# Kernel optimization log

Measured on AMD Instinct MI355X. Metric: run time of the kernel, lower is better.

The kernel has to match this reference:

```python
import jax, jax.numpy as jnp
import numpy as np

B, L, HID = 2, 2048, 4096
NH, NKV, HD = 16, 4, 64
BLOCK = 16
THETA = 8000000.0
EPS = 1e-6
NEG = jnp.finfo(jnp.float32).min


def _rope_tables(theta, L, hd):
    inv_freq = 1.0 / (theta ** (np.arange(0, hd, 2, dtype=np.float32) / hd))  # [hd/2]
    t = np.arange(L, dtype=np.float32)
    freqs = np.outer(t, inv_freq)                      # [L, hd/2]
    emb = np.concatenate([freqs, freqs], axis=-1)      # [L, hd]
    return jnp.asarray(np.cos(emb)), jnp.asarray(np.sin(emb))


def setup_inputs() -> dict:
    key = jax.random.key(0)
    k1, k2, k3 = jax.random.split(key, 3)
    hidden_states = jax.random.normal(k1, (B, L, HID), dtype=jnp.float32)
    Wqkv = jax.random.normal(k2, (HID, (NH + 2 * NKV) * HD), dtype=jnp.float32) * 0.006
    Wo = jax.random.normal(k3, (NH * HD, HID), dtype=jnp.float32) * 0.006
    q_norm_w = jnp.ones((HD,), dtype=jnp.float32)
    k_norm_w = jnp.ones((HD,), dtype=jnp.float32)
    # block-diagonal causal additive mask [1,1,L,L]
    idx = jnp.arange(L)
    same_block = (idx[:, None] // BLOCK) == (idx[None, :] // BLOCK)
    causal = idx[:, None] >= idx[None, :]
    attention_mask = jnp.where(same_block & causal, 0.0, NEG)[None, None].astype(jnp.float32)
    cos1, sin1 = _rope_tables(THETA, L, HD)
    cos = jnp.broadcast_to(cos1[None], (B, L, HD))
    sin = jnp.broadcast_to(sin1[None], (B, L, HD))
    return {"hidden_states": hidden_states, "attention_mask": attention_mask,
            "cos": cos, "sin": sin, "Wqkv": Wqkv, "Wo": Wo,
            "q_norm_w": q_norm_w, "k_norm_w": k_norm_w}


def _rms_norm(x, w):
    xf = x.astype(jnp.float32)
    var = jnp.mean(xf * xf, axis=-1, keepdims=True)
    return (xf * jax.lax.rsqrt(var + EPS)).astype(x.dtype) * w


def _rotate_half(x):
    x1, x2 = jnp.split(x, 2, axis=-1)
    return jnp.concatenate([-x2, x1], axis=-1)


def reference(hidden_states, attention_mask, cos, sin, Wqkv, Wo, q_norm_w, k_norm_w):
    Bc, Lc, _ = hidden_states.shape
    qkv = hidden_states @ Wqkv                                # [B,L,(NH+2NKV)*HD]
    qkv = qkv.reshape(Bc, Lc, NH + 2 * NKV, HD)
    q, k, v = jnp.split(qkv, [NH, NH + NKV], axis=2)
    q = q.transpose(0, 2, 1, 3)                               # [B,NH,L,HD]
    k = k.transpose(0, 2, 1, 3)                               # [B,NKV,L,HD]
    v = v.transpose(0, 2, 1, 3)
    q = _rms_norm(q, q_norm_w)
    k = _rms_norm(k, k_norm_w)
    c = cos[:, None]                                          # [B,1,L,HD]
    s = sin[:, None]
    q = q * c + _rotate_half(q) * s
    k = k * c + _rotate_half(k) * s
    groups = NH // NKV
    k = jnp.repeat(k, groups, axis=1)                         # [B,NH,L,HD]
    v = jnp.repeat(v, groups, axis=1)
    scale = 1.0 / jnp.sqrt(jnp.float32(HD))
    scores = jnp.einsum('bhqd,bhkd->bhqk', q, k) * scale + attention_mask
    probs = jax.nn.softmax(scores, axis=-1)
    out = jnp.einsum('bhqk,bhkd->bhqd', probs, v)             # [B,NH,L,HD]
    out = out.transpose(0, 2, 1, 3).reshape(Bc, Lc, NH * HD)
    return out @ Wo
```

## Files before the change

### kernel.cpp

```cpp
#include <hip/hip_runtime.h>
#include <hip/hip_bf16.h>
#include <cstdint>

#define B_SZ   2
#define L_SEQ  2048
#define HID    4096
#define NH     16
#define NKV    4
#define HD     64
#define NQKV   (NH + 2*NKV)
#define QKV_N  (NQKV*HD)
#define O_N    (NH*HD)
#define M_ROWS (B_SZ*L_SEQ)
#define EPSV   1e-6f

typedef __bf16  bf16x8_t  __attribute__((ext_vector_type(8)));
typedef float   f32x4_t   __attribute__((ext_vector_type(4)));
typedef unsigned short ushort8_t __attribute__((ext_vector_type(8)));

__device__ __forceinline__ unsigned short f2b(float f) {
    union { float f; uint32_t u; } v; v.f = f;
    uint32_t r = v.u + 0x7FFFu + ((v.u >> 16) & 1u);
    return (unsigned short)(r >> 16);
}
__device__ __forceinline__ float b2f(unsigned short u) {
    union { uint32_t u; float f; } v; v.u = ((uint32_t)u) << 16;
    return v.f;
}

__device__ __forceinline__ void gload_lds16(const void* g, void* l) {
    __builtin_amdgcn_global_load_lds(
        (__attribute__((address_space(1))) void*)(g),
        (__attribute__((address_space(3))) void*)(l),
        16, 0, 0);
}

#define BARF() do { asm volatile("" ::: "memory"); \
                    __builtin_amdgcn_s_barrier();  \
                    asm volatile("" ::: "memory"); } while (0)
#define LGKMW() asm volatile("s_waitcnt lgkmcnt(0)" ::: "memory")

template <int N> __device__ __forceinline__ void vmcnt_wait() {
    if constexpr (N == 4)       asm volatile("s_waitcnt vmcnt(4)"  ::: "memory");
    else if constexpr (N == 5)  asm volatile("s_waitcnt vmcnt(5)"  ::: "memory");
    else if constexpr (N == 6)  asm volatile("s_waitcnt vmcnt(6)"  ::: "memory");
    else if constexpr (N == 8)  asm volatile("s_waitcnt vmcnt(8)"  ::: "memory");
    else if constexpr (N == 12) asm volatile("s_waitcnt vmcnt(12)" ::: "memory");
    else                        asm volatile("s_waitcnt vmcnt(0)"  ::: "memory");
}

__global__ __launch_bounds__(256) void cvt_f32_bf16(const float* __restrict__ in,
                                                    unsigned short* __restrict__ out,
                                                    int n8) {
    int i = blockIdx.x * 256 + threadIdx.x;
    if (i >= n8) return;
    const float4* p = (const float4*)(in + (size_t)i * 8);
    float4 a = p[0], b = p[1];
    ushort8_t o;
    o[0]=f2b(a.x); o[1]=f2b(a.y); o[2]=f2b(a.z); o[3]=f2b(a.w);
    o[4]=f2b(b.x); o[5]=f2b(b.y); o[6]=f2b(b.z); o[7]=f2b(b.w);
    *(ushort8_t*)(out + (size_t)i * 8) = o;
}

__global__ __launch_bounds__(256) void transpose_both(const float* __restrict__ Wqkv,
                                                      unsigned short* __restrict__ WqkvT,
                                                      const float* __restrict__ Wo,
                                                      unsigned short* __restrict__ WoT) {
    __shared__ float t[32][33];
    const float* in;
    unsigned short* out;
    int R, C, bx, by;
    if (blockIdx.x < 6144) {
        in = Wqkv; out = WqkvT; R = HID; C = QKV_N;
        bx = blockIdx.x % 48; by = blockIdx.x / 48;
    } else {
        int b = blockIdx.x - 6144;
        in = Wo; out = WoT; R = O_N; C = HID;
        bx = b % 128; by = b / 128;
    }
    const int c0 = bx * 32;
    const int r0 = by * 32;
    const int tx = threadIdx.x & 31;
    const int ty = threadIdx.x >> 5;
    #pragma unroll
    for (int i = 0; i < 32; i += 8)
        t[ty + i][tx] = in[(size_t)(r0 + ty + i) * C + c0 + tx];
    __syncthreads();
    #pragma unroll
    for (int i = 0; i < 32; i += 8)
        out[(size_t)(c0 + ty + i) * R + r0 + tx] = f2b(t[tx][ty + i]);
}

template <int BM, int BN, int BK, int NBUF, int NWM, int NWN, bool OBF16, typename OutT>
__global__ __launch_bounds__(512, 2)
void gemm_sb(const unsigned short* __restrict__ A,
             const unsigned short* __restrict__ Bt,
             OutT* __restrict__ C, int M, int N, int K) {
    constexpr int WM    = BM / NWM;
    constexpr int WN    = BN / NWN;
    constexpr int AF    = WM / 16;
    constexpr int BF    = WN / 16;
    constexpr int KK    = BK / 32;
    constexpr int BUF   = (BM + BN) * BK;
    constexpr int ROWS  = 4096 / BK;
    constexpr int AR    = BM / ROWS;
    constexpr int BR    = BN / ROWS;
    constexpr int RNDS  = AR + BR;
    constexpr int DEPTH = NBUF - 2;

    __shared__ unsigned short smem[NBUF * BUF];

    const int tid  = threadIdx.x;
    const int lane = tid & 63;
    const int wave = tid >> 6;
    const int wm   = wave / NWN;
    const int wn   = wave % NWN;
    const int fr   = lane & 15;
    const int fq   = lane >> 4;

    const int nbx = N / BN;
    int bid = blockIdx.x;
    const int cpx = gridDim.x >> 3;
    bid = (bid & 7) * cpx + (bid >> 3);
    const int bx = bid % nbx, by = bid / nbx;
    const int m0 = by * BM, n0 = bx * BN;

    const int srow = tid / (BK / 8);
    const int sch  = tid & (BK / 8 - 1);
    const int ssw  = (BK == 64) ? (srow & 7) : ((srow >> 1) & 3);
    const int scs  = (sch ^ ssw) << 3;
    const unsigned short* gA = A  + (size_t)(m0 + srow) * K + scs;
    const unsigned short* gB = Bt + (size_t)(n0 + srow) * K + scs;

    const int frsw = (BK == 64) ? (fr & 7) : ((fr >> 1) & 3);

    f32x4_t acc[AF][BF];
    #pragma unroll
    for (int m = 0; m < AF; m++)
        #pragma unroll
        for (int n = 0; n < BF; n++)
            acc[m][n] = (f32x4_t){0.f, 0.f, 0.f, 0.f};

    const int NT = K / BK;

    auto STAGE = [&](int T) {
        const int pb = (T % NBUF) * BUF;
        #pragma unroll
        for (int q = 0; q < AR; ++q)
            gload_lds16(gA + (size_t)(q * ROWS) * K + (size_t)T * BK,
                        &smem[pb + q * 4096 + tid * 8]);
        #pragma unroll
        for (int q = 0; q < BR; ++q)
            gload_lds16(gB + (size_t)(q * ROWS) * K + (size_t)T * BK,
                        &smem[pb + BM * BK + q * 4096 + tid * 8]);
    };

    #pragma unroll
    for (int pt = 0; pt < NBUF - 1; ++pt) STAGE(pt);
    vmcnt_wait<DEPTH * RNDS>();

    for (int t = 0; t < NT; ++t) {
        const int sb = (t % NBUF) * BUF;
        BARF();

        #pragma unroll
        for (int kk = 0; kk < KK; ++kk) {
            const int cxk = (((kk * 4 + fq) ^ frsw)) << 3;
            bf16x8_t aF[AF], bF[BF];
            #pragma unroll
            for (int mm = 0; mm < AF; ++mm)
                aF[mm] = *(const bf16x8_t*)&smem[sb + (wm*WM + mm*16 + fr)*BK + cxk];
            #pragma unroll
            for (int nn = 0; nn < BF; ++nn)
                bF[nn] = *(const bf16x8_t*)&smem[sb + BM*BK + (wn*WN + nn*16 + fr)*BK + cxk];

            if (kk == 0 && t + NBUF - 1 < NT) STAGE(t + NBUF - 1);

            __builtin_amdgcn_s_setprio(1);
            #pragma unroll
            for (int mm = 0; mm < AF; ++mm)
                #pragma unroll
                for (int nn = 0; nn < BF; ++nn)
                    acc[mm][nn] = __builtin_amdgcn_mfma_f32_16x16x32_bf16(
                        aF[mm], bF[nn], acc[mm][nn], 0, 0, 0);
            __builtin_amdgcn_s_setprio(0);
        }

        if constexpr (DEPTH == 2) {
            if (t + 3 < NT)      { vmcnt_wait<2 * RNDS>(); }
            else if (t + 2 < NT) { vmcnt_wait<RNDS>(); }
            else if (t + 1 < NT) { vmcnt_wait<0>(); }
        } else {
            if (t + 2 < NT)      { vmcnt_wait<RNDS>(); }
            else if (t + 1 < NT) { vmcnt_wait<0>(); }
        }
    }

    const int crow = m0 + wm * WM + fq * 4;
    const int ccol = n0 + wn * WN + fr;
    #pragma unroll
    for (int m = 0; m < AF; m++)
        #pragma unroll
        for (int n = 0; n < BF; n++)
            #pragma unroll
            for (int rr = 0; rr < 4; rr++) {
                const size_t idx = (size_t)(crow + m*16 + rr) * N + ccol + n*16;
                if constexpr (OBF16) C[idx] = (OutT)f2b(acc[m][n][rr]);
                else                 C[idx] = (OutT)acc[m][n][rr];
            }
}

#define G2_BUF 32768

__global__ __launch_bounds__(512, 2)
void gemm2_8p(const unsigned short* __restrict__ A,
              const unsigned short* __restrict__ Bt,
              float* __restrict__ C) {
    constexpr int K     = O_N;
    constexpr int N     = HID;
    constexpr int NT    = K / 64;
    constexpr int NITER = NT / 2;

    __shared__ unsigned short smem[2 * G2_BUF];

    const int tid  = threadIdx.x;
    const int lane = tid & 63;
    const int wave = tid >> 6;
    const int wm   = wave >> 2;
    const int wn   = wave & 3;
    const int fr   = lane & 15;
    const int fq   = lane >> 4;

    const int nbx = N >> 8;
    int bid = blockIdx.x;
    const int cpx = gridDim.x >> 3;
    bid = (bid & 7) * cpx + (bid >> 3);
    const int bx = bid % nbx, by = bid / nbx;
    const int m0 = by << 8, n0 = bx << 8;

    const int srow = tid >> 3;
    const int scs  = ((tid & 7) ^ (srow & 7)) << 3;
    const unsigned short* gA = A  + (size_t)(m0 + srow) * K + scs;
    const unsigned short* gB = Bt + (size_t)(n0 + srow) * K + scs;
    const int frsw = fr & 7;

    f32x4_t acc[8][4];
    #pragma unroll
    for (int m = 0; m < 8; m++)
        #pragma unroll
        for (int n = 0; n < 4; n++)
            acc[m][n] = (f32x4_t){0.f, 0.f, 0.f, 0.f};

#define SA(T, q) gload_lds16(gA + (size_t)((q)*64)*K + (size_t)(T)*64, \
                             &smem[((T)&1)*G2_BUF + (q)*4096 + tid*8])
#define SB(T, q) gload_lds16(gB + (size_t)((q)*64)*K + (size_t)(T)*64, \
                             &smem[((T)&1)*G2_BUF + 16384 + (q)*4096 + tid*8])
#define RDA(T, MH, KI) { _Pragma("unroll") for (int mm = 0; mm < 4; ++mm) { \
    const int ro = ((T)&1)*G2_BUF + (wm*128 + (MH)*64 + mm*16 + fr)*64; \
    aF[mm] = *(const bf16x8_t*)&smem[ro + ((((KI)*4 + fq) ^ frsw) << 3)]; } }
#define RDB(T, KI, dst) { _Pragma("unroll") for (int nn = 0; nn < 4; ++nn) { \
    const int ro = ((T)&1)*G2_BUF + 16384 + (wn*64 + nn*16 + fr)*64; \
    dst[nn] = *(const bf16x8_t*)&smem[ro + ((((KI)*4 + fq) ^ frsw) << 3)]; } }
#define MM16(MH, BS) { __builtin_amdgcn_s_setprio(1); \
    _Pragma("unroll") for (int mm = 0; mm < 4; ++mm) \
    _Pragma("unroll") for (int nn = 0; nn < 4; ++nn) \
        acc[(MH)*4 + mm][nn] = __builtin_amdgcn_mfma_f32_16x16x32_bf16( \
            aF[mm], BS[nn], acc[(MH)*4 + mm][nn], 0, 0, 0); \
    __builtin_amdgcn_s_setprio(0); }

    SA(0,0); SA(0,1); SA(0,2); SA(0,3);
    SB(0,0); SB(0,1); SB(0,2); SB(0,3);
    SA(1,0); SA(1,2); SB(1,0); SB(1,1);
    vmcnt_wait<4>();
    BARF();

    for (int i = 0; i < NITER; ++i) {
        const int t0 = 2*i, t1 = 2*i + 1;
        bf16x8_t aF[4], b0[4], b1[4];

        RDA(t0, 0, 0); RDB(t0, 0, b0);
        SA(t1, 1); SA(t1, 3);
        BARF(); LGKMW(); MM16(0, b0); BARF();
        RDA(t0, 0, 1); RDB(t0, 1, b1);
        SB(t1, 2); SB(t1, 3);
        BARF(); LGKMW(); MM16(0, b1); BARF();
        RDA(t0, 1, 0);
        if (t0 + 2 < NT) { SA(t0 + 2, 0); SA(t0 + 2, 2); }
        BARF(); LGKMW(); MM16(1, b0); BARF();
        RDA(t0, 1, 1);
        if (t0 + 2 < NT) { SB(t0 + 2, 0); SB(t0 + 2, 1); }
        BARF(); LGKMW(); MM16(1, b1);
        if (i + 1 < NITER) { vmcnt_wait<4>(); } else { vmcnt_wait<0>(); }
        BARF();
        RDA(t1, 0, 0); RDB(t1, 0, b0);
        if (t0 + 2 < NT) { SA(t0 + 2, 1); SA(t0 + 2, 3); }
        BARF(); LGKMW(); MM16(0, b0); BARF();
        RDA(t1, 0, 1); RDB(t1, 1, b1);
        if (t0 + 2 < NT) { SB(t0 + 2, 2); SB(t0 + 2, 3); }
        BARF(); LGKMW(); MM16(0, b1); BARF();
        RDA(t1, 1, 0);
        if (t1 + 2 < NT) { SA(t1 + 2, 0); SA(t1 + 2, 2); }
        BARF(); LGKMW(); MM16(1, b0); BARF();
        RDA(t1, 1, 1);
        if (t1 + 2 < NT) { SB(t1 + 2, 0); SB(t1 + 2, 1); }
        BARF(); LGKMW(); MM16(1, b1);
        if (i + 1 < NITER) { vmcnt_wait<4>(); }
        BARF();
    }
#undef SA
#undef SB
#undef RDA
#undef RDB
#undef MM16

    const int crow = m0 + wm * 128 + fq * 4;
    const int ccol = n0 + wn * 64 + fr;
    #pragma unroll
    for (int m = 0; m < 8; m++)
        #pragma unroll
        for (int n = 0; n < 4; n++)
            #pragma unroll
            for (int rr = 0; rr < 4; rr++)
                C[(size_t)(crow + m*16 + rr) * N + ccol + n*16] = acc[m][n][rr];
}

__global__ __launch_bounds__(64) void attn_fused(const unsigned short* __restrict__ qkv,
                                                 const float* __restrict__ cosb,
                                                 const float* __restrict__ sinb,
                                                 const float* __restrict__ qw,
                                                 const float* __restrict__ kw,
                                                 unsigned short* __restrict__ out) {
    const int h    = blockIdx.x & (NH - 1);
    const int blk  = (blockIdx.x >> 4) & 127;
    const int b    = blockIdx.x >> 11;
    const int pos0 = blk * 16;
    const int kvh  = h >> 2;

    const int lane = threadIdx.x;
    const int r    = lane >> 2;
    const int qp   = lane & 3;
    const int d0   = qp * 16;

    __shared__ float qs[16][65];
    __shared__ float ks[16][65];
    __shared__ float vs[16][65];
    __shared__ float ps[16][17];

    const size_t rowb = ((size_t)(b * L_SEQ + pos0 + r)) * NQKV;
    const unsigned short* qptr = qkv + (rowb + h) * HD + d0;
    const unsigned short* kptr = qkv + (rowb + NH + kvh) * HD + d0;
    const unsigned short* vptr = qkv + (rowb + NH + NKV + kvh) * HD + d0;
    const size_t csrow = ((size_t)(b * L_SEQ + pos0 + r)) * HD + d0;

    float q[16], k[16], v[16], cs[16], sn[16];
    {
        ushort8_t q0 = *(const ushort8_t*)&qptr[0], q1 = *(const ushort8_t*)&qptr[8];
        ushort8_t k0 = *(const ushort8_t*)&kptr[0], k1 = *(const ushort8_t*)&kptr[8];
        ushort8_t v0 = *(const ushort8_t*)&vptr[0], v1 = *(const ushort8_t*)&vptr[8];
        #pragma unroll
        for (int i = 0; i < 8; i++) {
            q[i] = b2f(q0[i]); q[i+8] = b2f(q1[i]);
            k[i] = b2f(k0[i]); k[i+8] = b2f(k1[i]);
            v[i] = b2f(v0[i]); v[i+8] = b2f(v1[i]);
        }
        #pragma unroll
        for (int i = 0; i < 16; i += 4) {
            *(float4*)&cs[i] = *(const float4*)&cosb[csrow + i];
            *(float4*)&sn[i] = *(const float4*)&sinb[csrow + i];
        }
    }

    float sq = 0.f, sk = 0.f;
    #pragma unroll
    for (int i = 0; i < 16; i++) { sq += q[i]*q[i]; sk += k[i]*k[i]; }
    sq += __shfl_xor(sq, 1); sq += __shfl_xor(sq, 2);
    sk += __shfl_xor(sk, 1); sk += __shfl_xor(sk, 2);
    const float rq = rsqrtf(sq * (1.f / HD) + EPSV);
    const float rk = rsqrtf(sk * (1.f / HD) + EPSV);

    const float sgn = (qp < 2) ? -1.f : 1.f;
    #pragma unroll
    for (int i = 0; i < 16; i++) {
        float qn = q[i] * rq * qw[d0 + i];
        float kn = k[i] * rk * kw[d0 + i];
        float qo = __shfl_xor(qn, 2);
        float ko = __shfl_xor(kn, 2);
        qs[r][d0 + i] = qn * cs[i] + sgn * qo * sn[i];
        ks[r][d0 + i] = kn * cs[i] + sgn * ko * sn[i];
        vs[r][d0 + i] = v[i];
    }
    __syncthreads();

    float sc[4] = {0.f, 0.f, 0.f, 0.f};
    for (int d = 0; d < 64; d++) {
        const float qd = qs[r][d];
        sc[0] += qd * ks[qp     ][d];
        sc[1] += qd * ks[qp +  4][d];
        sc[2] += qd * ks[qp +  8][d];
        sc[3] += qd * ks[qp + 12][d];
    }
    #pragma unroll
    for (int cc = 0; cc < 4; cc++) {
        const int c = qp + cc * 4;
        sc[cc] = (c <= r) ? sc[cc] * 0.125f : -3.0e38f;
    }
    float mx = fmaxf(fmaxf(sc[0], sc[1]), fmaxf(sc[2], sc[3]));
    mx = fmaxf(mx, __shfl_xor(mx, 1));
    mx = fmaxf(mx, __shfl_xor(mx, 2));
    float e[4], sum = 0.f;
    #pragma unroll
    for (int cc = 0; cc < 4; cc++) { e[cc] = __expf(sc[cc] - mx); sum += e[cc]; }
    sum += __shfl_xor(sum, 1); sum += __shfl_xor(sum, 2);
    const float inv = 1.f / sum;
    #pragma unroll
    for (int cc = 0; cc < 4; cc++) ps[r][qp + cc * 4] = e[cc] * inv;
    __syncthreads();

    float o[16];
    #pragma unroll
    for (int i = 0; i < 16; i++) o[i] = 0.f;
    #pragma unroll
    for (int c = 0; c < 16; c++) {
        const float p = ps[r][c];
        #pragma unroll
        for (int i = 0; i < 16; i++) o[i] += p * vs[c][d0 + i];
    }

    __attribute__((aligned(16))) unsigned short ob[16];
    #pragma unroll
    for (int i = 0; i < 16; i++) ob[i] = f2b(o[i]);
    unsigned short* optr = out + (((size_t)(b * L_SEQ + pos0 + r) * NH + h) * HD) + d0;
    *(uint4*)optr       = *(uint4*)&ob[0];
    *((uint4*)optr + 1) = *(uint4*)&ob[8];
}

extern "C" void kernel_launch(void* const* d_in, const int* in_sizes, int n_in,
                              void* d_out, int out_size, void* d_ws, size_t ws_size,
                              hipStream_t stream) {
    const float* hid  = (const float*)d_in[0];
    const float* cosb = (const float*)d_in[2];
    const float* sinb = (const float*)d_in[3];
    const float* Wqkv = (const float*)d_in[4];
    const float* Wo   = (const float*)d_in[5];
    const float* qw   = (const float*)d_in[6];
    const float* kw   = (const float*)d_in[7];
    float* outp = (float*)d_out;

    char* ws = (char*)d_ws;
    unsigned short* Hb    = (unsigned short*)ws; ws += (size_t)M_ROWS * HID * 2;
    unsigned short* WqkvT = (unsigned short*)ws; ws += (size_t)QKV_N * HID * 2;
    unsigned short* WoT   = (unsigned short*)ws; ws += (size_t)HID * O_N * 2;
    unsigned short* qkvb  = (unsigned short*)ws; ws += (size_t)M_ROWS * QKV_N * 2;
    unsigned short* attnb = (unsigned short*)ws;

    {
        int n8 = (M_ROWS * HID) / 8;
        cvt_f32_bf16<<<(n8 + 255) / 256, 256, 0, stream>>>(hid, Hb, n8);
    }
    transpose_both<<<dim3(6144 + 4096), 256, 0, stream>>>(Wqkv, WqkvT, Wo, WoT);

    gemm_sb<128, 192, 64, 3, 2, 4, true, unsigned short>
        <<<dim3((M_ROWS / 128) * (QKV_N / 192)), 512, 0, stream>>>
        (Hb, WqkvT, qkvb, M_ROWS, QKV_N, HID);

    attn_fused<<<dim3(B_SZ * (L_SEQ / 16) * NH), 64, 0, stream>>>(qkvb, cosb, sinb, qw, kw, attnb);

    gemm2_8p<<<dim3((M_ROWS / 256) * (HID / 256)), 512, 0, stream>>>
        (attnb, WoT, outp);
}
```

Measured before the change: 144.5 us.

## Fuse fp32-to-bf16 activation conversion into QKV GEMM operand loads

Removes the separate activation conversion kernel and its bf16 workspace. The QKV GEMM now stages fp32 activations directly into LDS, double-buffered with a new XOR swizzle, and converts them to bf16 while building fragments. B stays triple-buffered, and the wait counts are retuned for the mixed buffering. The aim is to avoid writing and re-reading a 32 MB bf16 copy, at the cost of twice the A-tile global and LDS traffic plus conversion ALU work inside the GEMM loop.

```diff
diff --git a/kernel.cpp b/kernel.cpp
--- a/kernel.cpp
+++ b/kernel.cpp
@@ -41,25 +41,22 @@
 #define LGKMW() asm volatile("s_waitcnt lgkmcnt(0)" ::: "memory")
 
 template <int N> __device__ __forceinline__ void vmcnt_wait() {
-    if constexpr (N == 4)       asm volatile("s_waitcnt vmcnt(4)"  ::: "memory");
+    if constexpr (N == 3)       asm volatile("s_waitcnt vmcnt(3)"  ::: "memory");
+    else if constexpr (N == 4)  asm volatile("s_waitcnt vmcnt(4)"  ::: "memory");
     else if constexpr (N == 5)  asm volatile("s_waitcnt vmcnt(5)"  ::: "memory");
     else if constexpr (N == 6)  asm volatile("s_waitcnt vmcnt(6)"  ::: "memory");
+    else if constexpr (N == 7)  asm volatile("s_waitcnt vmcnt(7)"  ::: "memory");
     else if constexpr (N == 8)  asm volatile("s_waitcnt vmcnt(8)"  ::: "memory");
+    else if constexpr (N == 10) asm volatile("s_waitcnt vmcnt(10)" ::: "memory");
     else if constexpr (N == 12) asm volatile("s_waitcnt vmcnt(12)" ::: "memory");
     else                        asm volatile("s_waitcnt vmcnt(0)"  ::: "memory");
 }
 
-__global__ __launch_bounds__(256) void cvt_f32_bf16(const float* __restrict__ in,
-                                                    unsigned short* __restrict__ out,
-                                                    int n8) {
-    int i = blockIdx.x * 256 + threadIdx.x;
-    if (i >= n8) return;
-    const float4* p = (const float4*)(in + (size_t)i * 8);
-    float4 a = p[0], b = p[1];
-    ushort8_t o;
-    o[0]=f2b(a.x); o[1]=f2b(a.y); o[2]=f2b(a.z); o[3]=f2b(a.w);
-    o[4]=f2b(b.x); o[5]=f2b(b.y); o[6]=f2b(b.z); o[7]=f2b(b.w);
-    *(ushort8_t*)(out + (size_t)i * 8) = o;
+__device__ __forceinline__ bf16x8_t cvt8(float4 lo, float4 hi) {
+    bf16x8_t r;
+    r[0] = (__bf16)lo.x; r[1] = (__bf16)lo.y; r[2] = (__bf16)lo.z; r[3] = (__bf16)lo.w;
+    r[4] = (__bf16)hi.x; r[5] = (__bf16)hi.y; r[6] = (__bf16)hi.z; r[7] = (__bf16)hi.w;
+    return r;
 }
 
 __global__ __launch_bounds__(256) void transpose_both(const float* __restrict__ Wqkv,
@@ -91,48 +88,41 @@
         out[(size_t)(c0 + ty + i) * R + r0 + tx] = f2b(t[tx][ty + i]);
 }
 
-template <int BM, int BN, int BK, int NBUF, int NWM, int NWN, bool OBF16, typename OutT>
 __global__ __launch_bounds__(512, 2)
-void gemm_sb(const unsigned short* __restrict__ A,
-             const unsigned short* __restrict__ Bt,
-             OutT* __restrict__ C, int M, int N, int K) {
-    constexpr int WM    = BM / NWM;
-    constexpr int WN    = BN / NWN;
-    constexpr int AF    = WM / 16;
-    constexpr int BF    = WN / 16;
-    constexpr int KK    = BK / 32;
-    constexpr int BUF   = (BM + BN) * BK;
-    constexpr int ROWS  = 4096 / BK;
-    constexpr int AR    = BM / ROWS;
-    constexpr int BR    = BN / ROWS;
-    constexpr int RNDS  = AR + BR;
-    constexpr int DEPTH = NBUF - 2;
-
-    __shared__ unsigned short smem[NBUF * BUF];
+void gemm1_af32(const float* __restrict__ A32,
+                const unsigned short* __restrict__ Bt,
+                unsigned short* __restrict__ C) {
+    constexpr int AF = 4, BF = 3, Kd = HID, NT = HID / 64;
+
+    __shared__ unsigned short smem[69632];
 
     const int tid  = threadIdx.x;
     const int lane = tid & 63;
     const int wave = tid >> 6;
-    const int wm   = wave / NWN;
-    const int wn   = wave % NWN;
+    const int wm   = wave >> 2;
+    const int wn   = wave & 3;
     const int fr   = lane & 15;
     const int fq   = lane >> 4;
 
-    const int nbx = N / BN;
+    const int nbx = QKV_N / 192;
     int bid = blockIdx.x;
     const int cpx = gridDim.x >> 3;
     bid = (bid & 7) * cpx + (bid >> 3);
     const int bx = bid % nbx, by = bid / nbx;
-    const int m0 = by * BM, n0 = bx * BN;
-
-    const int srow = tid / (BK / 8);
-    const int sch  = tid & (BK / 8 - 1);
-    const int ssw  = (BK == 64) ? (srow & 7) : ((srow >> 1) & 3);
-    const int scs  = (sch ^ ssw) << 3;
-    const unsigned short* gA = A  + (size_t)(m0 + srow) * K + scs;
-    const unsigned short* gB = Bt + (size_t)(n0 + srow) * K + scs;
-
-    const int frsw = (BK == 64) ? (fr & 7) : ((fr >> 1) & 3);
+    const int m0 = by * 128, n0 = bx * 192;
+
+    float* As          = (float*)smem;
+    unsigned short* Bs = smem + 32768;
+
+    const int srA = tid >> 4;
+    const int scA = ((tid & 15) ^ ((srA & 7) << 1)) << 2;
+    const float* gA = A32 + (size_t)(m0 + srA) * Kd + scA;
+
+    const int srB = tid >> 3;
+    const int scB = ((tid & 7) ^ (srB & 7)) << 3;
+    const unsigned short* gB = Bt + (size_t)(n0 + srB) * Kd + scB;
+
+    const int frsw = fr & 7;
 
     f32x4_t acc[AF][BF];
     #pragma unroll
@@ -141,40 +131,50 @@
         for (int n = 0; n < BF; n++)
             acc[m][n] = (f32x4_t){0.f, 0.f, 0.f, 0.f};
 
-    const int NT = K / BK;
-
-    auto STAGE = [&](int T) {
-        const int pb = (T % NBUF) * BUF;
-        #pragma unroll
-        for (int q = 0; q < AR; ++q)
-            gload_lds16(gA + (size_t)(q * ROWS) * K + (size_t)T * BK,
-                        &smem[pb + q * 4096 + tid * 8]);
-        #pragma unroll
-        for (int q = 0; q < BR; ++q)
-            gload_lds16(gB + (size_t)(q * ROWS) * K + (size_t)T * BK,
-                        &smem[pb + BM * BK + q * 4096 + tid * 8]);
+    auto STAGE_A = [&](int T) {
+        float* dst = As + (T & 1) * 8192;
+        #pragma unroll
+        for (int q = 0; q < 4; ++q)
+            gload_lds16(gA + (size_t)(q * 32) * Kd + (size_t)T * 64,
+                        dst + q * 2048 + tid * 4);
     };
-
-    #pragma unroll
-    for (int pt = 0; pt < NBUF - 1; ++pt) STAGE(pt);
-    vmcnt_wait<DEPTH * RNDS>();
+    auto STAGE_B = [&](int T) {
+        unsigned short* dst = Bs + (T % 3) * 12288;
+        #pragma unroll
+        for (int q = 0; q < 3; ++q)
+            gload_lds16(gB + (size_t)(q * 64) * Kd + (size_t)T * 64,
+                        dst + q * 4096 + tid * 8);
+    };
+
+    STAGE_A(0); STAGE_B(0); STAGE_A(1); STAGE_B(1);
+    vmcnt_wait<7>();
 
     for (int t = 0; t < NT; ++t) {
-        const int sb = (t % NBUF) * BUF;
+        const float* Ab          = As + (t & 1) * 8192;
+        const unsigned short* Bb = Bs + (t % 3) * 12288;
         BARF();
 
         #pragma unroll
-        for (int kk = 0; kk < KK; ++kk) {
-            const int cxk = (((kk * 4 + fq) ^ frsw)) << 3;
+        for (int kk = 0; kk < 2; ++kk) {
             bf16x8_t aF[AF], bF[BF];
             #pragma unroll
-            for (int mm = 0; mm < AF; ++mm)
-                aF[mm] = *(const bf16x8_t*)&smem[sb + (wm*WM + mm*16 + fr)*BK + cxk];
+            for (int mm = 0; mm < AF; ++mm) {
+                const int ar = wm * 64 + mm * 16 + fr;
+                const int ac = ((kk * 8 + fq * 2) ^ (frsw << 1)) << 2;
+                float4 lo = *(const float4*)&Ab[ar * 64 + ac];
+                float4 hi = *(const float4*)&Ab[ar * 64 + ac + 4];
+                aF[mm] = cvt8(lo, hi);
+            }
             #pragma unroll
-            for (int nn = 0; nn < BF; ++nn)
-                bF[nn] = *(const bf16x8_t*)&smem[sb + BM*BK + (wn*WN + nn*16 + fr)*BK + cxk];
-
-            if (kk == 0 && t + NBUF - 1 < NT) STAGE(t + NBUF - 1);
+            for (int nn = 0; nn < BF; ++nn) {
+                const int cxk = ((kk * 4 + fq) ^ frsw) << 3;
+                bF[nn] = *(const bf16x8_t*)&Bb[(wn * 48 + nn * 16 + fr) * 64 + cxk];
+            }
+
+            if (kk == 0) {
+                if (t >= 1 && t + 1 < NT) STAGE_A(t + 1);
+                if (t + 2 < NT)           STAGE_B(t + 2);
+            }
 
             __builtin_amdgcn_s_setprio(1);
             #pragma unroll
@@ -186,28 +186,19 @@
             __builtin_amdgcn_s_setprio(0);
         }
 
-        if constexpr (DEPTH == 2) {
-            if (t + 3 < NT)      { vmcnt_wait<2 * RNDS>(); }
-            else if (t + 2 < NT) { vmcnt_wait<RNDS>(); }
-            else if (t + 1 < NT) { vmcnt_wait<0>(); }
-        } else {
-            if (t + 2 < NT)      { vmcnt_wait<RNDS>(); }
-            else if (t + 1 < NT) { vmcnt_wait<0>(); }
-        }
-    }
-
-    const int crow = m0 + wm * WM + fq * 4;
-    const int ccol = n0 + wn * WN + fr;
+        if (t + 2 < NT)      { vmcnt_wait<3>(); }
+        else if (t + 1 < NT) { vmcnt_wait<0>(); }
+    }
+
+    const int crow = m0 + wm * 64 + fq * 4;
+    const int ccol = n0 + wn * 48 + fr;
     #pragma unroll
     for (int m = 0; m < AF; m++)
         #pragma unroll
         for (int n = 0; n < BF; n++)
             #pragma unroll
-            for (int rr = 0; rr < 4; rr++) {
-                const size_t idx = (size_t)(crow + m*16 + rr) * N + ccol + n*16;
-                if constexpr (OBF16) C[idx] = (OutT)f2b(acc[m][n][rr]);
-                else                 C[idx] = (OutT)acc[m][n][rr];
-            }
+            for (int rr = 0; rr < 4; rr++)
+                C[(size_t)(crow + m*16 + rr) * QKV_N + ccol + n*16] = f2b(acc[m][n][rr]);
 }
 
 #define G2_BUF 32768
@@ -281,26 +272,33 @@
         RDA(t0, 0, 0); RDB(t0, 0, b0);
         SA(t1, 1); SA(t1, 3);
         BARF(); LGKMW(); MM16(0, b0); BARF();
+
         RDA(t0, 0, 1); RDB(t0, 1, b1);
         SB(t1, 2); SB(t1, 3);
         BARF(); LGKMW(); MM16(0, b1); BARF();
+
         RDA(t0, 1, 0);
         if (t0 + 2 < NT) { SA(t0 + 2, 0); SA(t0 + 2, 2); }
         BARF(); LGKMW(); MM16(1, b0); BARF();
+
         RDA(t0, 1, 1);
         if (t0 + 2 < NT) { SB(t0 + 2, 0); SB(t0 + 2, 1); }
         BARF(); LGKMW(); MM16(1, b1);
         if (i + 1 < NITER) { vmcnt_wait<4>(); } else { vmcnt_wait<0>(); }
         BARF();
+
         RDA(t1, 0, 0); RDB(t1, 0, b0);
         if (t0 + 2 < NT) { SA(t0 + 2, 1); SA(t0 + 2, 3); }
         BARF(); LGKMW(); MM16(0, b0); BARF();
+
         RDA(t1, 0, 1); RDB(t1, 1, b1);
         if (t0 + 2 < NT) { SB(t0 + 2, 2); SB(t0 + 2, 3); }
         BARF(); LGKMW(); MM16(0, b1); BARF();
+
         RDA(t1, 1, 0);
         if (t1 + 2 < NT) { SA(t1 + 2, 0); SA(t1 + 2, 2); }
         BARF(); LGKMW(); MM16(1, b0); BARF();
+
         RDA(t1, 1, 1);
         if (t1 + 2 < NT) { SB(t1 + 2, 0); SB(t1 + 2, 1); }
         BARF(); LGKMW(); MM16(1, b1);
@@ -447,21 +445,15 @@
     float* outp = (float*)d_out;
 
     char* ws = (char*)d_ws;
-    unsigned short* Hb    = (unsigned short*)ws; ws += (size_t)M_ROWS * HID * 2;
     unsigned short* WqkvT = (unsigned short*)ws; ws += (size_t)QKV_N * HID * 2;
     unsigned short* WoT   = (unsigned short*)ws; ws += (size_t)HID * O_N * 2;
     unsigned short* qkvb  = (unsigned short*)ws; ws += (size_t)M_ROWS * QKV_N * 2;
     unsigned short* attnb = (unsigned short*)ws;
 
-    {
-        int n8 = (M_ROWS * HID) / 8;
-        cvt_f32_bf16<<<(n8 + 255) / 256, 256, 0, stream>>>(hid, Hb, n8);
-    }
     transpose_both<<<dim3(6144 + 4096), 256, 0, stream>>>(Wqkv, WqkvT, Wo, WoT);
 
-    gemm_sb<128, 192, 64, 3, 2, 4, true, unsigned short>
-        <<<dim3((M_ROWS / 128) * (QKV_N / 192)), 512, 0, stream>>>
-        (Hb, WqkvT, qkvb, M_ROWS, QKV_N, HID);
+    gemm1_af32<<<dim3((M_ROWS / 128) * (QKV_N / 192)), 512, 0, stream>>>
+        (hid, WqkvT, qkvb);
 
     attn_fused<<<dim3(B_SZ * (L_SEQ / 16) * NH), 64, 0, stream>>>(qkvb, cosb, sinb, qw, kw, attnb);
 
```

Result: slower. 261.4 us (+80.9%).
